# Performance work log

Measured on AMD Instinct MI355X. Metric: run time of the kernel, lower is better.

## Reference

```python
import jax, jax.numpy as jnp
import numpy as np

N = 50000        # num nodes
E = 1600000      # num edges (avg degree 32)
DIN = 128        # dim_in
DOUT = 256       # dim_out
DA = 32          # dim_atten
SLOPE = 0.2      # leaky_relu negative slope


def setup_inputs() -> dict:
    key = jax.random.key(0)
    ks = jax.random.split(key, 9)
    x = jax.random.normal(ks[0], (N, DIN), dtype=jnp.float32)
    row = jax.random.randint(ks[1], (E,), 0, N, dtype=jnp.int32)
    col = jax.random.randint(ks[2], (E,), 0, N, dtype=jnp.int32)
    adj_val = jax.random.uniform(ks[3], (E,), dtype=jnp.float32)
    # learned params (Linear weights stored as [in, out] for x @ W)
    W_row = (jax.random.normal(ks[4], (DIN, DA)) / np.sqrt(DIN)).astype(jnp.float32)
    W_col = (jax.random.normal(ks[5], (DIN, DA)) / np.sqrt(DIN)).astype(jnp.float32)
    W_x = (jax.random.normal(ks[6], (DIN, DOUT)) / np.sqrt(DIN)).astype(jnp.float32)
    b_x = jnp.zeros((DOUT,), dtype=jnp.float32)
    return {"x": x, "row": row, "col": col, "adj_val": adj_val,
            "W_row": W_row, "W_col": W_col, "W_x": W_x, "b_x": b_x}


def reference(x, row, col, adj_val, W_row, W_col, W_x, b_x):
    # per-node attention projections
    a_row = x @ W_row                      # [N, DA]
    a_col = x @ W_col                      # [N, DA]
    # 'Multiply' attention: per-edge dot product scaled by rsqrt(DA)
    atten = jnp.sum(a_row[row] * a_col[col], axis=1) * jax.lax.rsqrt(jnp.float32(DA))  # [E]
    atten = jnp.where(atten >= 0, atten, SLOPE * atten)   # leaky_relu
    atten = jnp.exp(atten - jnp.max(atten))               # global-max-shifted exp
    # row-sum normalization (segment softmax denominator)
    deg = jax.ops.segment_sum(atten, row, num_segments=N)  # [N]
    atten = atten * (1.0 / (deg + 1e-15))[row]             # [E]
    # atten_combine == 'plus': average with original adjacency values
    vals = (adj_val + atten) * 0.5                         # [E]
    # sparse-dense matmul: out[i] = sum_{e: row[e]==i} vals[e] * x[col[e]]
    out = jax.ops.segment_sum(vals[:, None] * x[col], row, num_segments=N)  # [N, DIN]
    return out @ W_x + b_x                                 # [N, DOUT]
```

## Files before the change

kernel.cpp:

```cpp
#include <hip/hip_runtime.h>


#define DIN   128
#define DOUT  256
#define DA    32
#define SLOPE 0.2f
#define RSQRT_DA 0.17677669529663687f
#define BSH   6
#define BCAP  2560
#define CSTRIDE 32
#define NBMAX 800
#define PB_CHUNK 8192

typedef unsigned int uint;
typedef unsigned short ushort;
typedef __attribute__((ext_vector_type(8))) short bf16x8;
typedef __attribute__((ext_vector_type(4))) float f32x4;

static __device__ __forceinline__ ushort f2bf(float f) {
  const uint u = __float_as_uint(f);
  return (ushort)((u + 0x7fffu + ((u >> 16) & 1u)) >> 16);
}

__global__ __launch_bounds__(256) void wconv_kernel(
    const float* __restrict__ Wx, ushort* __restrict__ wxt,
    const float* __restrict__ Wr, const float* __restrict__ Wc,
    ushort* __restrict__ wrct, int* __restrict__ bcursor, int nb) {
  __shared__ ushort s[16][DIN];
  const int t = threadIdx.x;
  const int b = blockIdx.x;
  if (b < 16) {
    const int c0 = b * 16;
#pragma unroll
    for (int u = 0; u < 8; ++u) {
      const int k = u * 16 + (t >> 4);
      s[t & 15][k] = f2bf(Wx[(size_t)k * DOUT + c0 + (t & 15)]);
    }
    __syncthreads();
    const int c = t >> 4;
    const int kk = (t & 15) * 8;
    *(uint4*)(wxt + (size_t)(c0 + c) * DIN + kk) = *(const uint4*)&s[c][kk];
  } else if (b < 20) {
    const int c = (b - 16) * 16 + (t >> 4);
    const int k0 = (t & 15) * 8;
    const float* src = (c < DA) ? (Wr + c) : (Wc + (c - DA));
    ushort h[8];
#pragma unroll
    for (int j = 0; j < 8; ++j) h[j] = f2bf(src[(size_t)(k0 + j) * DA]);
    uint4 v;
    v.x = (uint)h[0] | ((uint)h[1] << 16);
    v.y = (uint)h[2] | ((uint)h[3] << 16);
    v.z = (uint)h[4] | ((uint)h[5] << 16);
    v.w = (uint)h[6] | ((uint)h[7] << 16);
    *(uint4*)(wrct + (size_t)c * DIN + k0) = v;
  } else {
    for (int i = t; i < nb; i += 256) bcursor[i * CSTRIDE] = i * BCAP;
  }
}

__global__ __launch_bounds__(256) void proj_kernel(
    const float* __restrict__ x, const ushort* __restrict__ wrct,
    float* __restrict__ a_row, ushort* __restrict__ a_colh,
    ushort* __restrict__ xh) {
  __shared__ ushort xb[16][136];
  const int t = threadIdx.x;
  const int node0 = blockIdx.x * 16;
  const float4* xg = (const float4*)(x + (size_t)node0 * DIN);
#pragma unroll
  for (int u = 0; u < 2; ++u) {
    const int f = t + u * 256;
    const float4 v = xg[f];
    ushort4 h;
    h.x = f2bf(v.x); h.y = f2bf(v.y); h.z = f2bf(v.z); h.w = f2bf(v.w);
    *(ushort4*)&xb[f >> 5][(f & 31) * 4] = h;
    ((ushort4*)(xh + (size_t)node0 * DIN))[f] = h;
  }
  __syncthreads();

  const int w = t >> 6;
  const int l = t & 63;
  const int lr = l & 15;
  const int lk = (l >> 4) * 8;
  f32x4 acc = {0.f, 0.f, 0.f, 0.f};
#pragma unroll
  for (int kk = 0; kk < 4; ++kk) {
    const bf16x8 a = *(const bf16x8*)&xb[lr][kk * 32 + lk];
    const bf16x8 bb =
        *(const bf16x8*)(wrct + (size_t)(w * 16 + lr) * DIN + kk * 32 + lk);
    acc = __builtin_amdgcn_mfma_f32_16x16x32_bf16(a, bb, acc, 0, 0, 0);
  }
  const int col = w * 16 + lr;
  const int r0 = (l >> 4) * 4;
#pragma unroll
  for (int r = 0; r < 4; ++r) {
    const int node = node0 + r0 + r;
    if (col < DA)
      a_row[(size_t)node * DA + col] = acc[r] * RSQRT_DA;
    else
      a_colh[(size_t)node * DA + (col - DA)] = f2bf(acc[r]);
  }
}

__global__ __launch_bounds__(512) void part_kernel(
    const int* __restrict__ row, const int* __restrict__ col,
    const float* __restrict__ adj, int* __restrict__ bcursor,
    int2* __restrict__ ibuf, int nb, int E) {
  __shared__ int hist[NBMAX];
  __shared__ int base[NBMAX];
  const int t = threadIdx.x;
  const int e0 = blockIdx.x * PB_CHUNK;
  for (int b = t; b < nb; b += 512) hist[b] = 0;
  __syncthreads();
  for (int u = 0; u < PB_CHUNK / 512; ++u) {
    const int e = e0 + u * 512 + t;
    if (e < E) atomicAdd(&hist[row[e] >> BSH], 1);
  }
  __syncthreads();
  for (int b = t; b < nb; b += 512) {
    const int c = hist[b];
    base[b] = c ? atomicAdd(&bcursor[b * CSTRIDE], c) : 0;
    hist[b] = 0;
  }
  __syncthreads();
  for (int u = 0; u < PB_CHUNK / 512; ++u) {
    const int e = e0 + u * 512 + t;
    if (e < E) {
      const int r = row[e];
      const int b = r >> BSH;
      const int pos = base[b] + atomicAdd(&hist[b], 1);
      ibuf[pos] = make_int2(((r & 63) << 16) | col[e], __float_as_int(adj[e]));
    }
  }
}

#define NODE_BODY(J)                                                    \
  {                                                                     \
    const int2 e = spk[w][half][(J)];                                   \
    const float pv = sp[w][half][(J)];                                  \
    const uint2 xv = xh2[(size_t)e.x * 32 + la];                        \
    const float av = __int_as_float(e.y);                               \
    const float f0 = __uint_as_float(xv.x << 16);                       \
    const float f1 = __uint_as_float(xv.x & 0xffff0000u);               \
    const float f2 = __uint_as_float(xv.y << 16);                       \
    const float f3 = __uint_as_float(xv.y & 0xffff0000u);               \
    aa0 += av * f0; aa1 += av * f1; aa2 += av * f2; aa3 += av * f3;     \
    ap0 += pv * f0; ap1 += pv * f1; ap2 += pv * f2; ap3 += pv * f3;     \
    deg += pv;                                                          \
  }

__global__ __launch_bounds__(512) void node_kernel(
    const uint* __restrict__ xh, const float* __restrict__ a_row,
    const ushort* __restrict__ a_colh, const int* __restrict__ bcursor,
    const int2* __restrict__ ibuf, ushort* __restrict__ feath, int n) {
  __shared__ int2  eL[BCAP];
  __shared__ int   cnt[64];
  __shared__ int   excl[65];
  __shared__ int2  spk[8][2][32];
  __shared__ float sp[8][2][32];
  __shared__ float s_ar[8][2][32];
  const int t = threadIdx.x;
  const int b = blockIdx.x;
  const int node0 = b << BSH;
  const int estart = b * BCAP;
  const int ecnt = bcursor[b * CSTRIDE] - estart;

  if (t < 64) cnt[t] = 0;
  __syncthreads();
  int2 myv[BCAP / 512];
#pragma unroll
  for (int u = 0; u < BCAP / 512; ++u) {
    const int e = u * 512 + t;
    if (e < ecnt) {
      myv[u] = ibuf[estart + e];
      atomicAdd(&cnt[myv[u].x >> 16], 1);
    }
  }
  __syncthreads();
  if (t < 64) {
    const int v = cnt[t];
    int inc = v;
#pragma unroll
    for (int ofs = 1; ofs < 64; ofs <<= 1) {
      const int o = __shfl_up(inc, ofs, 64);
      if (t >= ofs) inc += o;
    }
    excl[t] = inc - v;
    if (t == 63) excl[64] = inc;
    cnt[t] = 0;
  }
  __syncthreads();
#pragma unroll
  for (int u = 0; u < BCAP / 512; ++u) {
    const int e = u * 512 + t;
    if (e < ecnt) {
      const int rl = myv[u].x >> 16;
      const int pos = excl[rl] + atomicAdd(&cnt[rl], 1);
      eL[pos] = make_int2(myv[u].x & 0xffff, myv[u].y);
    }
  }
  __syncthreads();

  const int w = t >> 6;
  const int lane = t & 63;
  const int half = lane >> 5;
  const int la = lane & 31;
  const uint2* xh2 = (const uint2*)xh;

  for (int pp = 0; pp < 4; ++pp) {
    const int rl0 = (pp * 8 + w) * 2;
    const int i = node0 + rl0 + half;
    const int o0 = excl[rl0];
    const int o1 = excl[rl0 + 1];
    const int o2 = excl[rl0 + 2];
    const int d0 = o1 - o0, d1 = o2 - o1;
    const int myoff = half ? o1 : o0;
    const int myd = half ? d1 : d0;
    const int dmax = max(d0, d1);
    s_ar[w][half][la] = (i < n) ? a_row[(size_t)i * DA + la] : 0.f;

    float aa0 = 0.f, aa1 = 0.f, aa2 = 0.f, aa3 = 0.f;
    float ap0 = 0.f, ap1 = 0.f, ap2 = 0.f, ap3 = 0.f;
    float deg = 0.f;

    for (int base = 0; base < dmax; base += 32) {
      const int m = myd - base;
      if (la < m) {
        const int2 e = eL[myoff + base + la];
        spk[w][half][la] = e;
        const uint4* ac = (const uint4*)(a_colh + (size_t)e.x * DA);
        const float* ar = s_ar[w][half];
        float dot = 0.f;
#pragma unroll
        for (int k = 0; k < 4; ++k) {
          const uint4 q = ac[k];
          const float* a = ar + k * 8;
          dot += __uint_as_float(q.x << 16) * a[0] +
                 __uint_as_float(q.x & 0xffff0000u) * a[1] +
                 __uint_as_float(q.y << 16) * a[2] +
                 __uint_as_float(q.y & 0xffff0000u) * a[3] +
                 __uint_as_float(q.z << 16) * a[4] +
                 __uint_as_float(q.z & 0xffff0000u) * a[5] +
                 __uint_as_float(q.w << 16) * a[6] +
                 __uint_as_float(q.w & 0xffff0000u) * a[7];
        }
        const float lg = (dot >= 0.f) ? dot : SLOPE * dot;
        sp[w][half][la] = __expf(lg);
      } else {
        spk[w][half][la] = make_int2(0, 0);
        sp[w][half][la] = 0.f;
      }
      const int mmax = min(32, dmax - base);
      int j = 0;
      for (; j + 8 <= mmax; j += 8) {
#pragma unroll
        for (int u = 0; u < 8; ++u) NODE_BODY(j + u)
      }
      for (; j < mmax; ++j) NODE_BODY(j)
    }
    if (i < n) {
      const float inv = 0.5f / (deg + 1e-15f);
      ushort4 h;
      h.x = f2bf(0.5f * aa0 + inv * ap0);
      h.y = f2bf(0.5f * aa1 + inv * ap1);
      h.z = f2bf(0.5f * aa2 + inv * ap2);
      h.w = f2bf(0.5f * aa3 + inv * ap3);
      *(ushort4*)(feath + (size_t)i * DIN + la * 4) = h;
    }
  }
}

__global__ __launch_bounds__(256) void gemm_kernel(
    const ushort* __restrict__ feath, const ushort* __restrict__ wxt,
    const float* __restrict__ bx, float* __restrict__ out) {
  const int t = threadIdx.x;
  const int w = t >> 6;
  const int l = t & 63;
  const int row0 = blockIdx.x * 16;
  const int lr = l & 15;
  const int lk = (l >> 4) * 8;
  const int col0 = w * 64;

  f32x4 acc[4] = {f32x4{0.f, 0.f, 0.f, 0.f}, f32x4{0.f, 0.f, 0.f, 0.f},
                  f32x4{0.f, 0.f, 0.f, 0.f}, f32x4{0.f, 0.f, 0.f, 0.f}};
  const ushort* Abase = feath + (size_t)(row0 + lr) * DIN + lk;
#pragma unroll
  for (int kk = 0; kk < 4; ++kk) {
    const bf16x8 a = *(const bf16x8*)(Abase + kk * 32);
#pragma unroll
    for (int ct = 0; ct < 4; ++ct) {
      const bf16x8 b =
          *(const bf16x8*)(wxt + (size_t)(col0 + ct * 16 + lr) * DIN + kk * 32 + lk);
      acc[ct] = __builtin_amdgcn_mfma_f32_16x16x32_bf16(a, b, acc[ct], 0, 0, 0);
    }
  }
  const int crow0 = row0 + (l >> 4) * 4;
#pragma unroll
  for (int ct = 0; ct < 4; ++ct) {
    const int c = col0 + ct * 16 + lr;
    const float bv = bx[c];
#pragma unroll
    for (int r = 0; r < 4; ++r)
      out[(size_t)(crow0 + r) * DOUT + c] = acc[ct][r] + bv;
  }
}

extern "C" void kernel_launch(void* const* d_in, const int* in_sizes, int n_in,
                              void* d_out, int out_size, void* d_ws, size_t ws_size,
                              hipStream_t stream) {
  const float* x   = (const float*)d_in[0];
  const int*   row = (const int*)d_in[1];
  const int*   col = (const int*)d_in[2];
  const float* adj = (const float*)d_in[3];
  const float* Wr  = (const float*)d_in[4];
  const float* Wc  = (const float*)d_in[5];
  const float* Wx  = (const float*)d_in[6];
  const float* bx  = (const float*)d_in[7];
  float* out = (float*)d_out;

  const int n = in_sizes[0] / DIN;
  const int E = in_sizes[1];
  const int nb = (n + 63) >> BSH;

  int* w4 = (int*)d_ws;
  float* a_row   = (float*)w4;  w4 += (size_t)n * DA;
  ushort* feath  = (ushort*)w4; w4 += (size_t)n * DIN / 2;
  ushort* a_colh = (ushort*)w4; w4 += (size_t)n * DA / 2;
  uint*   xh     = (uint*)w4;   w4 += (size_t)n * DIN / 2;
  int2*   ibuf   = (int2*)w4;   w4 += (size_t)nb * BCAP * 2;
  int*    bcursor= w4;          w4 += (size_t)nb * CSTRIDE;
  ushort* wxt    = (ushort*)w4; w4 += (size_t)DOUT * DIN / 2;
  ushort* wrct   = (ushort*)w4;

  wconv_kernel<<<21, 256, 0, stream>>>(Wx, wxt, Wr, Wc, wrct, bcursor, nb);
  proj_kernel<<<n / 16, 256, 0, stream>>>(x, wrct, a_row, a_colh, (ushort*)xh);
  part_kernel<<<(E + PB_CHUNK - 1) / PB_CHUNK, 512, 0, stream>>>(
      row, col, adj, bcursor, ibuf, nb, E);
  node_kernel<<<nb, 512, 0, stream>>>(
      (const uint*)xh, a_row, a_colh, bcursor, ibuf, feath, n);
  gemm_kernel<<<n / 16, 256, 0, stream>>>(feath, wxt, bx, out);
}
```

Measured before the change: 265.3 us.

## Merge projection and partition kernels; fuse output GEMM into node aggregation

The projection kernel and the edge-partition kernel become one launch, with blocks split by blockIdx and sharing a union of LDS buffers, so the two independent phases run concurrently. The dense output GEMM is folded into node_kernel. Each block stages its 64 aggregated bf16 feature rows in LDS and multiplies them by W_x directly, which removes the feath round trip through global memory and one launch. The partition chunk size is doubled, and projection blocks now cover 32 nodes with tail guards. In exchange node_kernel uses more LDS (about 17KB extra), which may lower occupancy, and the GEMM in each block reads W_x from global memory.

```diff
diff --git a/kernel.cpp b/kernel.cpp
--- a/kernel.cpp
+++ b/kernel.cpp
@@ -10,7 +10,7 @@
 #define BCAP  2560
 #define CSTRIDE 32
 #define NBMAX 800
-#define PB_CHUNK 8192
+#define PB_CHUNK 16384
 
 typedef unsigned int uint;
 typedef unsigned short ushort;
@@ -58,22 +58,74 @@
   }
 }
 
-__global__ __launch_bounds__(256) void proj_kernel(
+__global__ __launch_bounds__(512) void super_kernel(
     const float* __restrict__ x, const ushort* __restrict__ wrct,
     float* __restrict__ a_row, ushort* __restrict__ a_colh,
-    ushort* __restrict__ xh) {
-  __shared__ ushort xb[16][136];
+    ushort* __restrict__ xh,
+    const int* __restrict__ row, const int* __restrict__ col,
+    const float* __restrict__ adj, int* __restrict__ bcursor,
+    int2* __restrict__ ibuf, int nb, int E, int npart, int n) {
+  __shared__ union {
+    struct { int hist[NBMAX]; int base[NBMAX]; } p;
+    ushort xb[32][136];
+  } sh;
   const int t = threadIdx.x;
-  const int node0 = blockIdx.x * 16;
+
+  if ((int)blockIdx.x < npart) {
+    int* hist = sh.p.hist;
+    int* base = sh.p.base;
+    const int e0 = blockIdx.x * PB_CHUNK;
+    for (int b = t; b < nb; b += 512) hist[b] = 0;
+    __syncthreads();
+    for (int u = 0; u < PB_CHUNK / 512; ++u) {
+      const int e = e0 + u * 512 + t;
+      if (e < E) atomicAdd(&hist[row[e] >> BSH], 1);
+    }
+    __syncthreads();
+    for (int b = t; b < nb; b += 512) {
+      const int c = hist[b];
+      base[b] = c ? atomicAdd(&bcursor[b * CSTRIDE], c) : 0;
+      hist[b] = 0;
+    }
+    __syncthreads();
+    for (int u = 0; u < PB_CHUNK / 512; ++u) {
+      const int e = e0 + u * 512 + t;
+      if (e < E) {
+        const int r = row[e];
+        const int b = r >> BSH;
+        const int pos = base[b] + atomicAdd(&hist[b], 1);
+        ibuf[pos] = make_int2(((r & 63) << 16) | col[e], __float_as_int(adj[e]));
+      }
+    }
+    return;
+  }
+
+  const int pb = blockIdx.x - npart;
+  const int node0 = pb * 32;
   const float4* xg = (const float4*)(x + (size_t)node0 * DIN);
-#pragma unroll
-  for (int u = 0; u < 2; ++u) {
-    const int f = t + u * 256;
-    const float4 v = xg[f];
-    ushort4 h;
-    h.x = f2bf(v.x); h.y = f2bf(v.y); h.z = f2bf(v.z); h.w = f2bf(v.w);
-    *(ushort4*)&xb[f >> 5][(f & 31) * 4] = h;
-    ((ushort4*)(xh + (size_t)node0 * DIN))[f] = h;
+  if (node0 + 32 <= n) {
+#pragma unroll
+    for (int u = 0; u < 2; ++u) {
+      const int f = t + u * 512;
+      const float4 v = xg[f];
+      ushort4 h;
+      h.x = f2bf(v.x); h.y = f2bf(v.y); h.z = f2bf(v.z); h.w = f2bf(v.w);
+      *(ushort4*)&sh.xb[f >> 5][(f & 31) * 4] = h;
+      ((ushort4*)(xh + (size_t)node0 * DIN))[f] = h;
+    }
+  } else {
+#pragma unroll
+    for (int u = 0; u < 2; ++u) {
+      const int f = t + u * 512;
+      const int nd = node0 + (f >> 5);
+      float4 v;
+      if (nd < n) v = xg[f];
+      else { v.x = 0.f; v.y = 0.f; v.z = 0.f; v.w = 0.f; }
+      ushort4 h;
+      h.x = f2bf(v.x); h.y = f2bf(v.y); h.z = f2bf(v.z); h.w = f2bf(v.w);
+      *(ushort4*)&sh.xb[f >> 5][(f & 31) * 4] = h;
+      if (nd < n) ((ushort4*)(xh + (size_t)node0 * DIN))[f] = h;
+    }
   }
   __syncthreads();
 
@@ -81,54 +133,26 @@
   const int l = t & 63;
   const int lr = l & 15;
   const int lk = (l >> 4) * 8;
+  const int h2 = w & 1;
+  const int q = w >> 1;
   f32x4 acc = {0.f, 0.f, 0.f, 0.f};
 #pragma unroll
   for (int kk = 0; kk < 4; ++kk) {
-    const bf16x8 a = *(const bf16x8*)&xb[lr][kk * 32 + lk];
+    const bf16x8 a = *(const bf16x8*)&sh.xb[h2 * 16 + lr][kk * 32 + lk];
     const bf16x8 bb =
-        *(const bf16x8*)(wrct + (size_t)(w * 16 + lr) * DIN + kk * 32 + lk);
+        *(const bf16x8*)(wrct + (size_t)(q * 16 + lr) * DIN + kk * 32 + lk);
     acc = __builtin_amdgcn_mfma_f32_16x16x32_bf16(a, bb, acc, 0, 0, 0);
   }
-  const int col = w * 16 + lr;
+  const int colq = q * 16 + lr;
   const int r0 = (l >> 4) * 4;
 #pragma unroll
   for (int r = 0; r < 4; ++r) {
-    const int node = node0 + r0 + r;
-    if (col < DA)
-      a_row[(size_t)node * DA + col] = acc[r] * RSQRT_DA;
-    else
-      a_colh[(size_t)node * DA + (col - DA)] = f2bf(acc[r]);
-  }
-}
-
-__global__ __launch_bounds__(512) void part_kernel(
-    const int* __restrict__ row, const int* __restrict__ col,
-    const float* __restrict__ adj, int* __restrict__ bcursor,
-    int2* __restrict__ ibuf, int nb, int E) {
-  __shared__ int hist[NBMAX];
-  __shared__ int base[NBMAX];
-  const int t = threadIdx.x;
-  const int e0 = blockIdx.x * PB_CHUNK;
-  for (int b = t; b < nb; b += 512) hist[b] = 0;
-  __syncthreads();
-  for (int u = 0; u < PB_CHUNK / 512; ++u) {
-    const int e = e0 + u * 512 + t;
-    if (e < E) atomicAdd(&hist[row[e] >> BSH], 1);
-  }
-  __syncthreads();
-  for (int b = t; b < nb; b += 512) {
-    const int c = hist[b];
-    base[b] = c ? atomicAdd(&bcursor[b * CSTRIDE], c) : 0;
-    hist[b] = 0;
-  }
-  __syncthreads();
-  for (int u = 0; u < PB_CHUNK / 512; ++u) {
-    const int e = e0 + u * 512 + t;
-    if (e < E) {
-      const int r = row[e];
-      const int b = r >> BSH;
-      const int pos = base[b] + atomicAdd(&hist[b], 1);
-      ibuf[pos] = make_int2(((r & 63) << 16) | col[e], __float_as_int(adj[e]));
+    const int node = node0 + h2 * 16 + r0 + r;
+    if (node < n) {
+      if (colq < DA)
+        a_row[(size_t)node * DA + colq] = acc[r] * RSQRT_DA;
+      else
+        a_colh[(size_t)node * DA + (colq - DA)] = f2bf(acc[r]);
     }
   }
 }
@@ -151,13 +175,15 @@
 __global__ __launch_bounds__(512) void node_kernel(
     const uint* __restrict__ xh, const float* __restrict__ a_row,
     const ushort* __restrict__ a_colh, const int* __restrict__ bcursor,
-    const int2* __restrict__ ibuf, ushort* __restrict__ feath, int n) {
+    const int2* __restrict__ ibuf, const ushort* __restrict__ wxt,
+    const float* __restrict__ bx, float* __restrict__ out, int n) {
   __shared__ int2  eL[BCAP];
   __shared__ int   cnt[64];
   __shared__ int   excl[65];
   __shared__ int2  spk[8][2][32];
   __shared__ float sp[8][2][32];
   __shared__ float s_ar[8][2][32];
+  __shared__ ushort sfeat[64][136];
   const int t = threadIdx.x;
   const int b = blockIdx.x;
   const int node0 = b << BSH;
@@ -257,50 +283,45 @@
       }
       for (; j < mmax; ++j) NODE_BODY(j)
     }
-    if (i < n) {
+    {
       const float inv = 0.5f / (deg + 1e-15f);
       ushort4 h;
       h.x = f2bf(0.5f * aa0 + inv * ap0);
       h.y = f2bf(0.5f * aa1 + inv * ap1);
       h.z = f2bf(0.5f * aa2 + inv * ap2);
       h.w = f2bf(0.5f * aa3 + inv * ap3);
-      *(ushort4*)(feath + (size_t)i * DIN + la * 4) = h;
-    }
-  }
-}
-
-__global__ __launch_bounds__(256) void gemm_kernel(
-    const ushort* __restrict__ feath, const ushort* __restrict__ wxt,
-    const float* __restrict__ bx, float* __restrict__ out) {
-  const int t = threadIdx.x;
-  const int w = t >> 6;
-  const int l = t & 63;
-  const int row0 = blockIdx.x * 16;
-  const int lr = l & 15;
-  const int lk = (l >> 4) * 8;
-  const int col0 = w * 64;
-
-  f32x4 acc[4] = {f32x4{0.f, 0.f, 0.f, 0.f}, f32x4{0.f, 0.f, 0.f, 0.f},
-                  f32x4{0.f, 0.f, 0.f, 0.f}, f32x4{0.f, 0.f, 0.f, 0.f}};
-  const ushort* Abase = feath + (size_t)(row0 + lr) * DIN + lk;
+      *(ushort4*)&sfeat[rl0 + half][la * 4] = h;
+    }
+  }
+  __syncthreads();
+
+  const int lr = lane & 15;
+  const int lk = (lane >> 4) * 8;
+  const int rt = (w & 3) * 16;
+  const int ct0 = (w >> 2) * 128;
+  f32x4 acc2[8];
+#pragma unroll
+  for (int ct = 0; ct < 8; ++ct) acc2[ct] = f32x4{0.f, 0.f, 0.f, 0.f};
 #pragma unroll
   for (int kk = 0; kk < 4; ++kk) {
-    const bf16x8 a = *(const bf16x8*)(Abase + kk * 32);
-#pragma unroll
-    for (int ct = 0; ct < 4; ++ct) {
-      const bf16x8 b =
-          *(const bf16x8*)(wxt + (size_t)(col0 + ct * 16 + lr) * DIN + kk * 32 + lk);
-      acc[ct] = __builtin_amdgcn_mfma_f32_16x16x32_bf16(a, b, acc[ct], 0, 0, 0);
-    }
-  }
-  const int crow0 = row0 + (l >> 4) * 4;
-#pragma unroll
-  for (int ct = 0; ct < 4; ++ct) {
-    const int c = col0 + ct * 16 + lr;
+    const bf16x8 a = *(const bf16x8*)&sfeat[rt + lr][kk * 32 + lk];
+#pragma unroll
+    for (int ct = 0; ct < 8; ++ct) {
+      const bf16x8 bb =
+          *(const bf16x8*)(wxt + (size_t)(ct0 + ct * 16 + lr) * DIN + kk * 32 + lk);
+      acc2[ct] = __builtin_amdgcn_mfma_f32_16x16x32_bf16(a, bb, acc2[ct], 0, 0, 0);
+    }
+  }
+  const int r0e = (lane >> 4) * 4;
+#pragma unroll
+  for (int ct = 0; ct < 8; ++ct) {
+    const int c = ct0 + ct * 16 + lr;
     const float bv = bx[c];
 #pragma unroll
-    for (int r = 0; r < 4; ++r)
-      out[(size_t)(crow0 + r) * DOUT + c] = acc[ct][r] + bv;
+    for (int r = 0; r < 4; ++r) {
+      const int node = node0 + rt + r0e + r;
+      if (node < n) out[(size_t)node * DOUT + c] = acc2[ct][r] + bv;
+    }
   }
 }
 
@@ -320,10 +341,11 @@
   const int n = in_sizes[0] / DIN;
   const int E = in_sizes[1];
   const int nb = (n + 63) >> BSH;
+  const int npart = (E + PB_CHUNK - 1) / PB_CHUNK;
+  const int nproj = (n + 31) / 32;
 
   int* w4 = (int*)d_ws;
   float* a_row   = (float*)w4;  w4 += (size_t)n * DA;
-  ushort* feath  = (ushort*)w4; w4 += (size_t)n * DIN / 2;
   ushort* a_colh = (ushort*)w4; w4 += (size_t)n * DA / 2;
   uint*   xh     = (uint*)w4;   w4 += (size_t)n * DIN / 2;
   int2*   ibuf   = (int2*)w4;   w4 += (size_t)nb * BCAP * 2;
@@ -332,10 +354,9 @@
   ushort* wrct   = (ushort*)w4;
 
   wconv_kernel<<<21, 256, 0, stream>>>(Wx, wxt, Wr, Wc, wrct, bcursor, nb);
-  proj_kernel<<<n / 16, 256, 0, stream>>>(x, wrct, a_row, a_colh, (ushort*)xh);
-  part_kernel<<<(E + PB_CHUNK - 1) / PB_CHUNK, 512, 0, stream>>>(
-      row, col, adj, bcursor, ibuf, nb, E);
+  super_kernel<<<npart + nproj, 512, 0, stream>>>(
+      x, wrct, a_row, a_colh, (ushort*)xh, row, col, adj, bcursor, ibuf,
+      nb, E, npart, n);
   node_kernel<<<nb, 512, 0, stream>>>(
-      (const uint*)xh, a_row, a_colh, bcursor, ibuf, feath, n);
-  gemm_kernel<<<n / 16, 256, 0, stream>>>(feath, wxt, bx, out);
-}
+      (const uint*)xh, a_row, a_colh, bcursor, ibuf, wxt, bx, out, n);
+}
```

Measured after the change: 272.1 us. 2.6% more time.
